# Performance work log

Hardware: AMD Instinct MI355X
Metric: run time of the kernel (lower is better)

Reference implementation:

```python
import jax, jax.numpy as jnp
import numpy as np

EPS = 1e-12  # matches torch F.normalize eps

def _l2norm(v, axis):
    n = jnp.sqrt(jnp.sum(v * v, axis=axis, keepdims=True))
    return v / jnp.maximum(n, EPS)

def setup_inputs() -> dict:
    key = jax.random.key(0)
    k1, k2, k3 = jax.random.split(key, 3)
    N, D, H, W, K = 64, 128, 60, 80, 64
    x = jax.random.normal(k1, (N, D, H, W), dtype=jnp.float32)
    conv_w = jax.random.normal(k2, (K, D), dtype=jnp.float32) * 0.1
    centroids = jax.random.uniform(k3, (K, D), dtype=jnp.float32)
    return {"x": x, "conv_w": conv_w, "centroids": centroids}

def reference(x, conv_w, centroids):
    N, D, H, W = x.shape
    K = conv_w.shape[0]
    # descriptor-wise L2 normalization over channel dim
    x = _l2norm(x, axis=1)
    xf = x.reshape(N, D, H * W)                       # [N, D, P]
    # 1x1 conv (no bias) == matmul over channels, then softmax over clusters
    logits = jnp.einsum('kd,ndp->nkp', conv_w, xf)    # [N, K, P]
    sa = jax.nn.softmax(logits, axis=1)               # [N, K, P]
    # vlad[n,k,:] = sum_p sa[n,k,p] * (xf[n,:,p] - centroids[k])
    agg = jnp.einsum('nkp,ndp->nkd', sa, xf)          # [N, K, D]
    vlad = agg - sa.sum(axis=-1)[..., None] * centroids[None]
    vlad = _l2norm(vlad, axis=2)                      # intra-normalization
    vlad = vlad.reshape(N, K * D)
    vlad = _l2norm(vlad, axis=1)                      # global L2 norm
    return vlad
```

## Files before the change

kernel.cpp:

```cpp
#include <hip/hip_runtime.h>
#include <hip/hip_bf16.h>
#include <hip/hip_fp16.h>
#include <math.h>

#define NN 64
#define DD 128
#define PP 4800
#define KK 64
#define BPN 15
#define PB  320
#define CP  64
#define NCH 5

#define TSTR 72

#define PAGG_SZ  ((size_t)NN * BPN * KK * DD)
#define PSSUM_SZ ((size_t)NN * BPN * KK)

typedef __attribute__((ext_vector_type(8))) short bf16x8;
typedef __attribute__((ext_vector_type(4))) float f32x4;
typedef __attribute__((ext_vector_type(2))) unsigned int u32x2;
typedef __attribute__((address_space(3))) const unsigned short lds_cus;

__device__ __forceinline__ unsigned pk2(float a, float b) {
  union { __hip_bfloat162 h2; unsigned u; } cv;
  cv.h2 = __float22bfloat162_rn(make_float2(a, b));
  return cv.u;
}

#define TR_READ(dst, addr, imm)                                          \
  asm volatile("ds_read_b64_tr_b16 %0, %1 offset:" #imm                  \
               : "=v"(dst) : "v"(addr))

__global__ __launch_bounds__(256, 2) void main_kernel(const float* __restrict__ x,
                                                      const float* __restrict__ conv_w,
                                                      __half* __restrict__ pagg,
                                                      float* __restrict__ pssum) {
  __shared__ __align__(16) unsigned short xdp[128 * TSTR];
  __shared__ __align__(16) unsigned short sa_t[64 * TSTR];
  __shared__ float red_s[256];

  const int b = blockIdx.x;
  const int n = b / BPN, sl = b % BPN;
  const int t = threadIdx.x, lane = t & 63, wv = t >> 6;
  const int lq = lane >> 4, ll = lane & 15;
  const int pb = t & 7, db = t >> 3;

  bf16x8 wf[4][4];
#pragma unroll
  for (int kt = 0; kt < 4; ++kt)
#pragma unroll
    for (int ks = 0; ks < 4; ++ks) {
      const float* wp = conv_w + (kt * 16 + ll) * DD + ks * 32 + lq * 8;
      float4 a = *(const float4*)wp;
      float4 c = *(const float4*)(wp + 4);
      union { unsigned u[4]; bf16x8 v; } cv;
      cv.u[0] = pk2(a.x, a.y); cv.u[1] = pk2(a.z, a.w);
      cv.u[2] = pk2(c.x, c.y); cv.u[3] = pk2(c.z, c.w);
      wf[kt][ks] = cv.v;
    }

  const float* xb = x + (size_t)n * DD * PP + (size_t)(4 * db) * PP + sl * PB + 8 * pb;

  float4 pf[8];
#pragma unroll
  for (int r = 0; r < 4; ++r) {
    pf[2 * r]     = *(const float4*)(xb + (size_t)r * PP);
    pf[2 * r + 1] = *(const float4*)(xb + (size_t)r * PP + 4);
  }

  f32x4 acc[8];
#pragma unroll
  for (int i = 0; i < 8; ++i) acc[i] = (f32x4){0.f, 0.f, 0.f, 0.f};
  float ssacc[16];
#pragma unroll
  for (int i = 0; i < 16; ++i) ssacc[i] = 0.f;

  const int wbase = (db * 4 + (pb >> 1)) * TSTR + 8 * (pb & 1);
  const unsigned trbase =
      (unsigned)(size_t)((lds_cus*)xdp + (8 * lq + wv) * TSTR + 4 * ll);
  const unsigned atrbase =
      (unsigned)(size_t)((lds_cus*)sa_t + (8 * lq + wv) * TSTR + 4 * ll);
  const int g2base = ((ll >> 2) * 4 + (lq >> 1)) * TSTR + (ll & 3) * 16 + (lq & 1) * 8;
  const int prow_ = wv * 16 + ll;
  const int sabase = ((prow_ >> 2) * 4) * TSTR + (prow_ & 3) * 16 + lq * 4;

  for (int c = 0; c < NCH; ++c) {
    float4 cur[8];
#pragma unroll
    for (int i = 0; i < 8; ++i) cur[i] = pf[i];
    if (c + 1 < NCH) {
      const float* xc = xb + (c + 1) * CP;
#pragma unroll
      for (int r = 0; r < 4; ++r) {
        pf[2 * r]     = *(const float4*)(xc + (size_t)r * PP);
        pf[2 * r + 1] = *(const float4*)(xc + (size_t)r * PP + 4);
      }
    }

    float sq[8];
#pragma unroll
    for (int h = 0; h < 2; ++h)
#pragma unroll
      for (int j = 0; j < 4; ++j) {
        float s = 0.f;
#pragma unroll
        for (int r = 0; r < 4; ++r) {
          float v = (&cur[2 * r + h].x)[j];
          s = fmaf(v, v, s);
        }
        sq[4 * h + j] = s;
      }
#pragma unroll
    for (int i = 0; i < 8; ++i) {
      int d = __builtin_amdgcn_update_dpp(0, __float_as_int(sq[i]), 0x128, 0xF, 0xF, false);
      sq[i] += __int_as_float(d);
    }
    float v4[4];
#pragma unroll
    for (int j = 0; j < 4; ++j) v4[j] = (lane & 8) ? sq[j + 4] : sq[j];
#pragma unroll
    for (int j = 0; j < 4; ++j) {
      v4[j] += __shfl_xor(v4[j], 16);
      v4[j] += __shfl_xor(v4[j], 32);
    }

    __syncthreads();

    if (lane < 16) {
      float4 o = {v4[0], v4[1], v4[2], v4[3]};
      *(float4*)&red_s[wv * 64 + 8 * (lane & 7) + 4 * (lane >> 3)] = o;
    }

#pragma unroll
    for (int r = 0; r < 4; ++r) {
      const float4& a = cur[2 * r];
      const float4& c2 = cur[2 * r + 1];
      uint4 o = {pk2(a.x, a.y), pk2(a.z, a.w), pk2(c2.x, c2.y), pk2(c2.z, c2.w)};
      *(uint4*)&xdp[wbase + r * 16] = o;
    }
    __syncthreads();

    {
      u32x2 trv[8];
      TR_READ(trv[0], trbase, 0);
      TR_READ(trv[1], trbase, 576);
      TR_READ(trv[2], trbase, 4608);
      TR_READ(trv[3], trbase, 5184);
      TR_READ(trv[4], trbase, 9216);
      TR_READ(trv[5], trbase, 9792);
      TR_READ(trv[6], trbase, 13824);
      TR_READ(trv[7], trbase, 14400);
      asm volatile("s_waitcnt lgkmcnt(0)" ::: "memory");
      __builtin_amdgcn_sched_barrier(0);

      f32x4 lg[4];
#pragma unroll
      for (int kt = 0; kt < 4; ++kt) lg[kt] = (f32x4){0.f, 0.f, 0.f, 0.f};
#pragma unroll
      for (int ks = 0; ks < 4; ++ks) {
        union { unsigned u[4]; bf16x8 v; } bu;
        bu.u[0] = trv[2 * ks].x;
        bu.u[1] = trv[2 * ks].y;
        bu.u[2] = trv[2 * ks + 1].x;
        bu.u[3] = trv[2 * ks + 1].y;
        bf16x8 bfrag = bu.v;
#pragma unroll
        for (int kt = 0; kt < 4; ++kt)
          lg[kt] = __builtin_amdgcn_mfma_f32_16x16x32_bf16(wf[kt][ks], bfrag, lg[kt], 0, 0, 0);
      }
      float sum4 = red_s[prow_] + red_s[64 + prow_] + red_s[128 + prow_] + red_s[192 + prow_];
      float iv = 1.0f / fmaxf(sqrtf(sum4), 1e-12f);
      float vals[16];
#pragma unroll
      for (int kt = 0; kt < 4; ++kt)
#pragma unroll
        for (int r = 0; r < 4; ++r)
          vals[kt * 4 + r] = __expf(lg[kt][r] * iv);
      float s0 = (vals[0] + vals[1]) + (vals[2] + vals[3]);
      float s1 = (vals[4] + vals[5]) + (vals[6] + vals[7]);
      float s2 = (vals[8] + vals[9]) + (vals[10] + vals[11]);
      float s3 = (vals[12] + vals[13]) + (vals[14] + vals[15]);
      float se = (s0 + s1) + (s2 + s3);
      se += __shfl_xor(se, 16);
      se += __shfl_xor(se, 32);
      float rinv = 1.0f / se;
      float r2 = rinv * iv;
#pragma unroll
      for (int kt = 0; kt < 4; ++kt) {
        float e0 = vals[kt * 4 + 0], e1 = vals[kt * 4 + 1];
        float e2 = vals[kt * 4 + 2], e3 = vals[kt * 4 + 3];
        ssacc[kt * 4 + 0] += e0 * rinv;
        ssacc[kt * 4 + 1] += e1 * rinv;
        ssacc[kt * 4 + 2] += e2 * rinv;
        ssacc[kt * 4 + 3] += e3 * rinv;
        *(uint2*)&sa_t[sabase + kt * TSTR] =
            make_uint2(pk2(e0 * r2, e1 * r2), pk2(e2 * r2, e3 * r2));
      }
    }
    __syncthreads();

    {
      u32x2 av[4];
      TR_READ(av[0], atrbase, 0);
      TR_READ(av[1], atrbase, 576);
      TR_READ(av[2], atrbase, 4608);
      TR_READ(av[3], atrbase, 5184);
      asm volatile("s_waitcnt lgkmcnt(0)" ::: "memory");
      __builtin_amdgcn_sched_barrier(0);
#pragma unroll
      for (int ks = 0; ks < 2; ++ks) {
        union { unsigned u[4]; bf16x8 v; } au;
        au.u[0] = av[2 * ks].x;
        au.u[1] = av[2 * ks].y;
        au.u[2] = av[2 * ks + 1].x;
        au.u[3] = av[2 * ks + 1].y;
        bf16x8 afrag = au.v;
#pragma unroll
        for (int dt = 0; dt < 8; ++dt) {
          bf16x8 bfrag = *(const bf16x8*)&xdp[g2base + dt * (16 * TSTR) + ks * (2 * TSTR)];
          acc[dt] = __builtin_amdgcn_mfma_f32_16x16x32_bf16(afrag, bfrag, acc[dt], 0, 0, 0);
        }
      }
    }
  }

  {
    __half* base = pagg + (size_t)(n * BPN + sl) * (KK * DD);
#pragma unroll
    for (int dt = 0; dt < 8; ++dt)
#pragma unroll
      for (int r = 0; r < 4; ++r)
        base[(16 * wv + 4 * lq + r) * DD + dt * 16 + ll] = __float2half(acc[dt][r]);
  }
#pragma unroll
  for (int i = 0; i < 16; ++i) {
    float s = ssacc[i];
    s += __shfl_xor(s, 1);
    s += __shfl_xor(s, 2);
    s += __shfl_xor(s, 4);
    s += __shfl_xor(s, 8);
    if (ll == 0) red_s[wv * 64 + (i >> 2) * 16 + lq * 4 + (i & 3)] = s;
  }
  __syncthreads();
  if (t < 64)
    pssum[(n * BPN + sl) * KK + t] =
        red_s[t] + red_s[64 + t] + red_s[128 + t] + red_s[192 + t];
}

__global__ __launch_bounds__(256) void ep_kernel(const __half* __restrict__ pagg,
                                                 const float* __restrict__ pssum,
                                                 const float* __restrict__ cent,
                                                 float* __restrict__ out) {
  const int blk = blockIdx.x;
  const int n = blk >> 3, kg = blk & 7;
  const int t = threadIdx.x;
  const int kl = t >> 5, c32 = t & 31;
  const int k = kg * 8 + kl;
  const size_t off = (size_t)k * DD + c32 * 4;

  const __half* base = pagg + (size_t)n * BPN * (KK * DD) + off;
  float4 a = {0.f, 0.f, 0.f, 0.f};
  for (int s = 0; s < BPN; ++s) {
    uint2 u = *(const uint2*)(base + (size_t)s * (KK * DD));
    __half2 h0 = *(const __half2*)&u.x;
    __half2 h1 = *(const __half2*)&u.y;
    float2 f0 = __half22float2(h0);
    float2 f1 = __half22float2(h1);
    a.x += f0.x; a.y += f0.y; a.z += f1.x; a.w += f1.y;
  }
  float sk = 0.f;
  for (int s = 0; s < BPN; ++s) sk += pssum[(n * BPN + s) * KK + k];

  float4 c4 = *(const float4*)(cent + off);
  float4 v;
  v.x = fmaf(-sk, c4.x, a.x);
  v.y = fmaf(-sk, c4.y, a.y);
  v.z = fmaf(-sk, c4.z, a.z);
  v.w = fmaf(-sk, c4.w, a.w);

  float ss = v.x * v.x + v.y * v.y + v.z * v.z + v.w * v.w;
  ss += __shfl_xor(ss, 1);
  ss += __shfl_xor(ss, 2);
  ss += __shfl_xor(ss, 4);
  ss += __shfl_xor(ss, 8);
  ss += __shfl_xor(ss, 16);
  float scale = 0.125f / fmaxf(sqrtf(ss), 1e-12f);
  v.x *= scale; v.y *= scale; v.z *= scale; v.w *= scale;
  *(float4*)(out + (size_t)n * (KK * DD) + off) = v;
}

extern "C" void kernel_launch(void* const* d_in, const int* in_sizes, int n_in,
                              void* d_out, int out_size, void* d_ws, size_t ws_size,
                              hipStream_t stream) {
  const float* x      = (const float*)d_in[0];
  const float* conv_w = (const float*)d_in[1];
  const float* cent   = (const float*)d_in[2];
  float* out = (float*)d_out;
  float* ws  = (float*)d_ws;

  __half* pagg = (__half*)ws;
  float* pssum = ws + PAGG_SZ / 2;

  main_kernel<<<NN * BPN, 256, 0, stream>>>(x, conv_w, pagg, pssum);
  ep_kernel<<<NN * 8, 256, 0, stream>>>(pagg, pssum, cent, out);
}
```

Before: 246.6 us.

## Fuse epilogue into main kernel via last-block atomic counter per sample

Removes the separate epilogue kernel. Each main-kernel block increments a per-sample atomic counter after a threadfence, and the last of the 15 blocks for a sample reduces the fp16 partial aggregates, subtracts the centroid term and applies both normalisations. This saves one kernel launch and lets the epilogue for early samples overlap with later main blocks. In exchange, the tail work for each sample runs in a single 256-thread block with 32 floats per thread, and a tiny zero kernel is added to reset the counters.

```diff
diff --git a/kernel.cpp b/kernel.cpp
--- a/kernel.cpp
+++ b/kernel.cpp
@@ -32,13 +32,21 @@
   asm volatile("ds_read_b64_tr_b16 %0, %1 offset:" #imm                  \
                : "=v"(dst) : "v"(addr))
 
+__global__ void zero_kernel(int* __restrict__ cnt) {
+  cnt[threadIdx.x] = 0;
+}
+
 __global__ __launch_bounds__(256, 2) void main_kernel(const float* __restrict__ x,
                                                       const float* __restrict__ conv_w,
+                                                      const float* __restrict__ cent,
                                                       __half* __restrict__ pagg,
-                                                      float* __restrict__ pssum) {
+                                                      float* __restrict__ pssum,
+                                                      int* __restrict__ cnt,
+                                                      float* __restrict__ out) {
   __shared__ __align__(16) unsigned short xdp[128 * TSTR];
   __shared__ __align__(16) unsigned short sa_t[64 * TSTR];
   __shared__ float red_s[256];
+  __shared__ int lastf;
 
   const int b = blockIdx.x;
   const int n = b / BPN, sl = b % BPN;
@@ -246,48 +254,59 @@
   if (t < 64)
     pssum[(n * BPN + sl) * KK + t] =
         red_s[t] + red_s[64 + t] + red_s[128 + t] + red_s[192 + t];
-}
-
-__global__ __launch_bounds__(256) void ep_kernel(const __half* __restrict__ pagg,
-                                                 const float* __restrict__ pssum,
-                                                 const float* __restrict__ cent,
-                                                 float* __restrict__ out) {
-  const int blk = blockIdx.x;
-  const int n = blk >> 3, kg = blk & 7;
-  const int t = threadIdx.x;
-  const int kl = t >> 5, c32 = t & 31;
-  const int k = kg * 8 + kl;
-  const size_t off = (size_t)k * DD + c32 * 4;
-
-  const __half* base = pagg + (size_t)n * BPN * (KK * DD) + off;
-  float4 a = {0.f, 0.f, 0.f, 0.f};
-  for (int s = 0; s < BPN; ++s) {
-    uint2 u = *(const uint2*)(base + (size_t)s * (KK * DD));
-    __half2 h0 = *(const __half2*)&u.x;
-    __half2 h1 = *(const __half2*)&u.y;
-    float2 f0 = __half22float2(h0);
-    float2 f1 = __half22float2(h1);
-    a.x += f0.x; a.y += f0.y; a.z += f1.x; a.w += f1.y;
-  }
-  float sk = 0.f;
-  for (int s = 0; s < BPN; ++s) sk += pssum[(n * BPN + s) * KK + k];
-
-  float4 c4 = *(const float4*)(cent + off);
-  float4 v;
-  v.x = fmaf(-sk, c4.x, a.x);
-  v.y = fmaf(-sk, c4.y, a.y);
-  v.z = fmaf(-sk, c4.z, a.z);
-  v.w = fmaf(-sk, c4.w, a.w);
-
-  float ss = v.x * v.x + v.y * v.y + v.z * v.z + v.w * v.w;
-  ss += __shfl_xor(ss, 1);
-  ss += __shfl_xor(ss, 2);
-  ss += __shfl_xor(ss, 4);
-  ss += __shfl_xor(ss, 8);
-  ss += __shfl_xor(ss, 16);
-  float scale = 0.125f / fmaxf(sqrtf(ss), 1e-12f);
-  v.x *= scale; v.y *= scale; v.z *= scale; v.w *= scale;
-  *(float4*)(out + (size_t)n * (KK * DD) + off) = v;
+
+  __threadfence();
+  __syncthreads();
+  if (t == 0) lastf = (atomicAdd(&cnt[n], 1) == BPN - 1);
+  __syncthreads();
+  if (!lastf) return;
+  __threadfence();
+
+  {
+    const int k = t >> 2, dseg = (t & 3) * 32;
+    float va[32];
+#pragma unroll
+    for (int i = 0; i < 32; ++i) va[i] = 0.f;
+    const __half* pb2 = pagg + (size_t)n * (BPN * KK * DD) + (size_t)k * DD + dseg;
+    for (int s = 0; s < BPN; ++s) {
+      const uint4* q = (const uint4*)(pb2 + (size_t)s * (KK * DD));
+      union { uint4 v[4]; unsigned u[16]; } Q;
+      Q.v[0] = q[0]; Q.v[1] = q[1]; Q.v[2] = q[2]; Q.v[3] = q[3];
+#pragma unroll
+      for (int j = 0; j < 16; ++j) {
+        float2 f = __half22float2(*(const __half2*)&Q.u[j]);
+        va[2 * j]     += f.x;
+        va[2 * j + 1] += f.y;
+      }
+    }
+    float sk = 0.f;
+    for (int s = 0; s < BPN; ++s) sk += pssum[(n * BPN + s) * KK + k];
+
+    const float* cp = cent + k * DD + dseg;
+    float ss = 0.f;
+#pragma unroll
+    for (int i = 0; i < 8; ++i) {
+      float4 c4 = *(const float4*)(cp + 4 * i);
+      float v0 = fmaf(-sk, c4.x, va[4 * i + 0]);
+      float v1 = fmaf(-sk, c4.y, va[4 * i + 1]);
+      float v2 = fmaf(-sk, c4.z, va[4 * i + 2]);
+      float v3 = fmaf(-sk, c4.w, va[4 * i + 3]);
+      va[4 * i + 0] = v0; va[4 * i + 1] = v1;
+      va[4 * i + 2] = v2; va[4 * i + 3] = v3;
+      ss = fmaf(v0, v0, ss); ss = fmaf(v1, v1, ss);
+      ss = fmaf(v2, v2, ss); ss = fmaf(v3, v3, ss);
+    }
+    ss += __shfl_xor(ss, 1);
+    ss += __shfl_xor(ss, 2);
+    float scale = 0.125f / fmaxf(sqrtf(ss), 1e-12f);
+    float* op = out + (size_t)n * (KK * DD) + (size_t)k * DD + dseg;
+#pragma unroll
+    for (int i = 0; i < 8; ++i) {
+      float4 w = {va[4 * i] * scale, va[4 * i + 1] * scale,
+                  va[4 * i + 2] * scale, va[4 * i + 3] * scale};
+      *(float4*)(op + 4 * i) = w;
+    }
+  }
 }
 
 extern "C" void kernel_launch(void* const* d_in, const int* in_sizes, int n_in,
@@ -301,7 +320,8 @@
 
   __half* pagg = (__half*)ws;
   float* pssum = ws + PAGG_SZ / 2;
-
-  main_kernel<<<NN * BPN, 256, 0, stream>>>(x, conv_w, pagg, pssum);
-  ep_kernel<<<NN * 8, 256, 0, stream>>>(pagg, pssum, cent, out);
+  int* cnt     = (int*)(pssum + PSSUM_SZ);
+
+  zero_kernel<<<1, NN, 0, stream>>>(cnt);
+  main_kernel<<<NN * BPN, 256, 0, stream>>>(x, conv_w, cent, pagg, pssum, cnt, out);
 }
```

New measurement: 490.1 us. 98.7% more time.

## Stage conv weights in LDS and reorder prefetch to raise occupancy

Applied to the files above, without the earlier changes.

The bf16 conv weight fragments are no longer held in 64 VGPRs per thread. They are written once into a padded LDS tile and read per MFMA, and launch bounds go from 2 to 3 blocks per SIMD. The chunk loop now computes norms and stores from the prefetch registers directly before issuing the next prefetch, which removes the copy into a separate cur buffer. This trades register pressure for extra LDS reads per chunk and about 17KB more LDS per block, which may itself limit occupancy.

```diff
diff --git a/kernel.cpp b/kernel.cpp
--- a/kernel.cpp
+++ b/kernel.cpp
@@ -12,6 +12,7 @@
 #define CP  64
 #define NCH 5
 
+#define WT  136
 #define TSTR 72
 
 #define PAGG_SZ  ((size_t)NN * BPN * KK * DD)
@@ -32,10 +33,11 @@
   asm volatile("ds_read_b64_tr_b16 %0, %1 offset:" #imm                  \
                : "=v"(dst) : "v"(addr))
 
-__global__ __launch_bounds__(256, 2) void main_kernel(const float* __restrict__ x,
+__global__ __launch_bounds__(256, 3) void main_kernel(const float* __restrict__ x,
                                                       const float* __restrict__ conv_w,
                                                       __half* __restrict__ pagg,
                                                       float* __restrict__ pssum) {
+  __shared__ __align__(16) unsigned short w_s[KK * WT];
   __shared__ __align__(16) unsigned short xdp[128 * TSTR];
   __shared__ __align__(16) unsigned short sa_t[64 * TSTR];
   __shared__ float red_s[256];
@@ -46,19 +48,18 @@
   const int lq = lane >> 4, ll = lane & 15;
   const int pb = t & 7, db = t >> 3;
 
-  bf16x8 wf[4][4];
-#pragma unroll
-  for (int kt = 0; kt < 4; ++kt)
-#pragma unroll
-    for (int ks = 0; ks < 4; ++ks) {
-      const float* wp = conv_w + (kt * 16 + ll) * DD + ks * 32 + lq * 8;
-      float4 a = *(const float4*)wp;
-      float4 c = *(const float4*)(wp + 4);
-      union { unsigned u[4]; bf16x8 v; } cv;
-      cv.u[0] = pk2(a.x, a.y); cv.u[1] = pk2(a.z, a.w);
-      cv.u[2] = pk2(c.x, c.y); cv.u[3] = pk2(c.z, c.w);
-      wf[kt][ks] = cv.v;
-    }
+  {
+    int k = t >> 2, h = t & 3;
+    const float* wp = conv_w + k * DD + h * 32;
+    unsigned short* dst = &w_s[k * WT + h * 32];
+#pragma unroll
+    for (int i = 0; i < 4; ++i) {
+      float4 a = *(const float4*)(wp + 8 * i);
+      float4 c = *(const float4*)(wp + 8 * i + 4);
+      uint4 o = {pk2(a.x, a.y), pk2(a.z, a.w), pk2(c.x, c.y), pk2(c.z, c.w)};
+      *(uint4*)&dst[8 * i] = o;
+    }
+  }
 
   const float* xb = x + (size_t)n * DD * PP + (size_t)(4 * db) * PP + sl * PB + 8 * pb;
 
@@ -86,9 +87,48 @@
   const int sabase = ((prow_ >> 2) * 4) * TSTR + (prow_ & 3) * 16 + lq * 4;
 
   for (int c = 0; c < NCH; ++c) {
-    float4 cur[8];
-#pragma unroll
-    for (int i = 0; i < 8; ++i) cur[i] = pf[i];
+    float sq[8];
+#pragma unroll
+    for (int h = 0; h < 2; ++h)
+#pragma unroll
+      for (int j = 0; j < 4; ++j) {
+        float s = 0.f;
+#pragma unroll
+        for (int r = 0; r < 4; ++r) {
+          float v = (&pf[2 * r + h].x)[j];
+          s = fmaf(v, v, s);
+        }
+        sq[4 * h + j] = s;
+      }
+#pragma unroll
+    for (int i = 0; i < 8; ++i) {
+      int d = __builtin_amdgcn_update_dpp(0, __float_as_int(sq[i]), 0x128, 0xF, 0xF, false);
+      sq[i] += __int_as_float(d);
+    }
+    float v4[4];
+#pragma unroll
+    for (int j = 0; j < 4; ++j) v4[j] = (lane & 8) ? sq[j + 4] : sq[j];
+#pragma unroll
+    for (int j = 0; j < 4; ++j) {
+      v4[j] += __shfl_xor(v4[j], 16);
+      v4[j] += __shfl_xor(v4[j], 32);
+    }
+
+    __syncthreads();
+
+    if (lane < 16) {
+      float4 o = {v4[0], v4[1], v4[2], v4[3]};
+      *(float4*)&red_s[wv * 64 + 8 * (lane & 7) + 4 * (lane >> 3)] = o;
+    }
+
+#pragma unroll
+    for (int r = 0; r < 4; ++r) {
+      const float4& a = pf[2 * r];
+      const float4& c2 = pf[2 * r + 1];
+      uint4 o = {pk2(a.x, a.y), pk2(a.z, a.w), pk2(c2.x, c2.y), pk2(c2.z, c2.w)};
+      *(uint4*)&xdp[wbase + r * 16] = o;
+    }
+
     if (c + 1 < NCH) {
       const float* xc = xb + (c + 1) * CP;
 #pragma unroll
@@ -96,48 +136,6 @@
         pf[2 * r]     = *(const float4*)(xc + (size_t)r * PP);
         pf[2 * r + 1] = *(const float4*)(xc + (size_t)r * PP + 4);
       }
-    }
-
-    float sq[8];
-#pragma unroll
-    for (int h = 0; h < 2; ++h)
-#pragma unroll
-      for (int j = 0; j < 4; ++j) {
-        float s = 0.f;
-#pragma unroll
-        for (int r = 0; r < 4; ++r) {
-          float v = (&cur[2 * r + h].x)[j];
-          s = fmaf(v, v, s);
-        }
-        sq[4 * h + j] = s;
-      }
-#pragma unroll
-    for (int i = 0; i < 8; ++i) {
-      int d = __builtin_amdgcn_update_dpp(0, __float_as_int(sq[i]), 0x128, 0xF, 0xF, false);
-      sq[i] += __int_as_float(d);
-    }
-    float v4[4];
-#pragma unroll
-    for (int j = 0; j < 4; ++j) v4[j] = (lane & 8) ? sq[j + 4] : sq[j];
-#pragma unroll
-    for (int j = 0; j < 4; ++j) {
-      v4[j] += __shfl_xor(v4[j], 16);
-      v4[j] += __shfl_xor(v4[j], 32);
-    }
-
-    __syncthreads();
-
-    if (lane < 16) {
-      float4 o = {v4[0], v4[1], v4[2], v4[3]};
-      *(float4*)&red_s[wv * 64 + 8 * (lane & 7) + 4 * (lane >> 3)] = o;
-    }
-
-#pragma unroll
-    for (int r = 0; r < 4; ++r) {
-      const float4& a = cur[2 * r];
-      const float4& c2 = cur[2 * r + 1];
-      uint4 o = {pk2(a.x, a.y), pk2(a.z, a.w), pk2(c2.x, c2.y), pk2(c2.z, c2.w)};
-      *(uint4*)&xdp[wbase + r * 16] = o;
     }
     __syncthreads();
 
@@ -166,8 +164,10 @@
         bu.u[3] = trv[2 * ks + 1].y;
         bf16x8 bfrag = bu.v;
 #pragma unroll
-        for (int kt = 0; kt < 4; ++kt)
-          lg[kt] = __builtin_amdgcn_mfma_f32_16x16x32_bf16(wf[kt][ks], bfrag, lg[kt], 0, 0, 0);
+        for (int kt = 0; kt < 4; ++kt) {
+          bf16x8 afrag = *(const bf16x8*)&w_s[(kt * 16 + ll) * WT + ks * 32 + lq * 8];
+          lg[kt] = __builtin_amdgcn_mfma_f32_16x16x32_bf16(afrag, bfrag, lg[kt], 0, 0, 0);
+        }
       }
       float sum4 = red_s[prow_] + red_s[64 + prow_] + red_s[128 + prow_] + red_s[192 + prow_];
       float iv = 1.0f / fmaxf(sqrtf(sum4), 1e-12f);
```

Measured after the change: 246.6 us. No clear change (-0.0%).
